# Optimization experiments

Hardware: AMD Instinct MI355X
Metric: run time of the kernel (lower is better)

Reference implementation:

```python
import jax, jax.numpy as jnp
import numpy as np

BERT = 178  # BERT_VECTOR_SIZE
WLEN = 20   # letters per word (dim1 = WLEN + BERT)


def _lstm(x, h0, c0, Wih, Whh, bih, bhh):
    """PyTorch-convention LSTM (gate order i,f,g,o). x: [B,T,D] -> outputs [B,T,H]."""
    xg = jnp.einsum('btd,gd->btg', x, Wih) + bih + bhh  # precompute input projections

    def step(carry, xt):
        h, c = carry
        g = xt + h @ Whh.T
        i, f, gg, o = jnp.split(g, 4, axis=-1)
        c = jax.nn.sigmoid(f) * c + jax.nn.sigmoid(i) * jnp.tanh(gg)
        h = jax.nn.sigmoid(o) * jnp.tanh(c)
        return (h, c), h

    _, hs = jax.lax.scan(step, (h0, c0), jnp.swapaxes(xg, 0, 1))
    return jnp.swapaxes(hs, 0, 1)  # [B,T,H]


def setup_inputs() -> dict:
    key = jax.random.key(0)
    ks = jax.random.split(key, 32)
    B, S, L = 32, 64, 50          # batch, sentence_length, number_of_letters
    Hs, Hm, D, O = 128, 256, 128, 32  # secondary_hidden, main_hidden, word_dims, output_size
    NW = B * S
    T = WLEN + BERT
    Din = D + BERT                # sentence LSTM input size = 306
    s = 0.05
    rn = lambda k, sh: jax.random.normal(k, sh, dtype=jnp.float32)
    return {
        'X': rn(ks[0], (B, S, T, L)),
        'h0w': rn(ks[1], (NW, Hs)), 'c0w': rn(ks[2], (NW, Hs)),
        'h0f': rn(ks[3], (B, Hm)), 'c0f': rn(ks[4], (B, Hm)),
        'h0b': rn(ks[5], (B, Hm)), 'c0b': rn(ks[6], (B, Hm)),
        'Wih_w': rn(ks[7], (4 * Hs, L)) * s, 'Whh_w': rn(ks[8], (4 * Hs, Hs)) * s,
        'bih_w': rn(ks[9], (4 * Hs,)) * s, 'bhh_w': rn(ks[10], (4 * Hs,)) * s,
        'Wl': rn(ks[11], (D, Hs)) * s, 'bl': rn(ks[12], (D,)) * s,
        'Wih_f': rn(ks[13], (4 * Hm, Din)) * s, 'Whh_f': rn(ks[14], (4 * Hm, Hm)) * s,
        'bih_f': rn(ks[15], (4 * Hm,)) * s, 'bhh_f': rn(ks[16], (4 * Hm,)) * s,
        'Wih_b': rn(ks[17], (4 * Hm, Din)) * s, 'Whh_b': rn(ks[18], (4 * Hm, Hm)) * s,
        'bih_b': rn(ks[19], (4 * Hm,)) * s, 'bhh_b': rn(ks[20], (4 * Hm,)) * s,
        'Wo': rn(ks[21], (O, 2 * Hm)) * s, 'bo': rn(ks[22], (O,)) * s,
    }


def reference(X, h0w, c0w, h0f, c0f, h0b, c0b,
              Wih_w, Whh_w, bih_w, bhh_w, Wl, bl,
              Wih_f, Whh_f, bih_f, bhh_f,
              Wih_b, Whh_b, bih_b, bhh_b, Wo, bo):
    B, S = X.shape[0], X.shape[1]
    L = X.shape[-1]
    NW = B * S
    Xw = X.reshape(NW, -1, L)            # [NW, WLEN+BERT, L]
    letters = Xw[:, :WLEN, :]            # [NW, WLEN, L]
    bert = Xw[:, -BERT:, 0]              # vectorized replacement of the double loop

    out_w = _lstm(letters, h0w, c0w, Wih_w, Whh_w, bih_w, bhh_w)
    word_rep = out_w[:, -1, :] @ Wl.T + bl        # [NW, D]
    word_rep = jnp.concatenate([word_rep, bert], axis=1)  # [NW, D+BERT]
    sentences = word_rep.reshape(B, S, -1)

    out_f = _lstm(sentences, h0f, c0f, Wih_f, Whh_f, bih_f, bhh_f)
    out_b = _lstm(sentences[:, ::-1, :], h0b, c0b, Wih_b, Whh_b, bih_b, bhh_b)[:, ::-1, :]
    out = jnp.concatenate([out_f, out_b], axis=-1)  # [B, S, 2*Hm]

    words = out.reshape(NW, -1)
    tags = words @ Wo.T + bo
    return jax.nn.softmax(tags, axis=1)
```

## Files before the change

kernel.cpp:

```cpp
#include <hip/hip_runtime.h>
#include <cstdint>
#include <cstddef>

#define DI static __device__ __forceinline__

using half_t  = _Float16;
using half2_t = __attribute__((ext_vector_type(2))) _Float16;
using half8_t = __attribute__((ext_vector_type(8))) _Float16;
using f32x4_t = __attribute__((ext_vector_type(4))) float;

DI uint32_t pack2(float a, float b){ half2_t h; h[0]=(half_t)a; h[1]=(half_t)b; return __builtin_bit_cast(uint32_t,h); }
DI uint16_t f16b(float a){ return __builtin_bit_cast(uint16_t,(half_t)a); }
DI float lo16(uint32_t u){ half2_t h=__builtin_bit_cast(half2_t,u); return (float)h[0]; }
DI float hi16(uint32_t u){ half2_t h=__builtin_bit_cast(half2_t,u); return (float)h[1]; }
DI float fdot2(uint32_t w, uint32_t x, float acc){
  return __builtin_amdgcn_fdot2(__builtin_bit_cast(half2_t,w), __builtin_bit_cast(half2_t,x), acc, false);
}
DI float sigm(float x){ return __builtin_amdgcn_rcpf(1.f + __expf(-x)); }
DI float tanhf_(float x){ return 1.f - 2.f*__builtin_amdgcn_rcpf(__expf(2.f*x)+1.f); }

#define SROW 308

#define N0 32768
#define N1 16384
#define N2 8192
#define N3 512
#define N4 262144
#define N5 313344
#define N6 2048
#define N7 8192
#define N8 364544
#define NTOT (N0+N1+N2+N3+N4+N5+N6+N7+N8)

__global__ void k_prep(const float* __restrict__ X,
                       const float* __restrict__ Wih_w, const float* __restrict__ Whh_w,
                       const float* __restrict__ bih_w, const float* __restrict__ bhh_w,
                       const float* __restrict__ Wl,
                       const float* __restrict__ Wih_f, const float* __restrict__ Whh_f,
                       const float* __restrict__ bih_f, const float* __restrict__ bhh_f,
                       const float* __restrict__ Wih_b, const float* __restrict__ Whh_b,
                       const float* __restrict__ bih_b, const float* __restrict__ bhh_b,
                       const float* __restrict__ Wo,
                       uint32_t* __restrict__ wWsw, uint32_t* __restrict__ wWxw,
                       uint32_t* __restrict__ wWlf, float* __restrict__ wbsw,
                       uint32_t* __restrict__ wWs, uint32_t* __restrict__ wWihs,
                       float* __restrict__ wbss, uint32_t* __restrict__ wWo,
                       float* __restrict__ sent)
{
  for (int i = blockIdx.x*blockDim.x + threadIdx.x; i < NTOT; i += gridDim.x*blockDim.x) {
    int id = i;
    if (id < N0) {
      int kp = id & 63, ng = id >> 6;
      int w = ng>>6, g = (ng>>4)&3, jl = ng&15;
      const float* s = Whh_w + (size_t)(g*128 + w*16 + jl)*128 + 2*kp;
      wWsw[id] = pack2(s[0], s[1]);
    } else if ((id -= N0) < N1) {
      int kp = id & 31, ng = id >> 5;
      int w = ng>>6, g = (ng>>4)&3, jl = ng&15;
      if (kp < 25) {
        const float* s = Wih_w + (size_t)(g*128 + w*16 + jl)*50 + 2*kp;
        wWxw[id] = pack2(s[0], s[1]);
      } else wWxw[id] = 0u;
    } else if ((id -= N1) < N2) {
      int kp = id & 63, d = id >> 6;
      const float* s = Wl + (size_t)d*128 + 2*kp;
      wWlf[id] = pack2(s[0], s[1]);
    } else if ((id -= N2) < N3) {
      int g = id & 3, j = id>>2;
      wbsw[id] = bih_w[g*128+j] + bhh_w[g*128+j];
    } else if ((id -= N3) < N4) {
      int kp = id & 127, ng = (id>>7)&1023, dir = id>>17;
      int w = ng>>7, g = (ng>>5)&3, jl = ng&31;
      int row = g*256 + w*32 + jl;
      const float* s = (dir ? Whh_b : Whh_f) + (size_t)row*256 + 2*kp;
      wWs[id] = pack2(s[0], s[1]);
    } else if ((id -= N4) < N5) {
      int dir = id >= 156672; int r = id - dir*156672;
      int g = r & 3, j = (r>>2)&255, kp = r>>10;
      const float* s = (dir ? Wih_b : Wih_f) + (size_t)(g*256+j)*306 + 2*kp;
      wWihs[id] = pack2(s[0], s[1]);
    } else if ((id -= N5) < N6) {
      int g = id & 3, j = (id>>2)&255, dir = id>>10;
      int row = g*256+j;
      wbss[id] = dir ? (bih_b[row]+bhh_b[row]) : (bih_f[row]+bhh_f[row]);
    } else if ((id -= N6) < N7) {
      int o = id & 31, kp = id>>5;
      const float* s = Wo + (size_t)o*512 + 2*kp;
      wWo[id] = pack2(s[0], s[1]);
    } else { id -= N7;
      int wg = id / 178, ii = id % 178;
      sent[(size_t)wg*SROW + 128 + ii] = X[(size_t)wg*9900 + (20+ii)*50];
    }
  }
}

__global__ __launch_bounds__(512, 2) void k_word(
    const float* __restrict__ X, const float* __restrict__ h0w, const float* __restrict__ c0w,
    const uint32_t* __restrict__ wWsw, const uint32_t* __restrict__ wWxw,
    const float* __restrict__ wbsw, const uint32_t* __restrict__ wWlf,
    const float* __restrict__ bl, float* __restrict__ sent)
{
  __shared__ __align__(16) uint32_t lets[11520];
  __shared__ __align__(16) uint16_t hbuf[2][2176];
  const int tid = threadIdx.x;
  const int wave = tid >> 6, lane = tid & 63;
  const int l15 = lane & 15, l4 = lane >> 4;
  const int wg0 = blockIdx.x * 16;

  uint4 Bh[4][4], Bx[4][2];
  #pragma unroll
  for (int g = 0; g < 4; ++g) {
    int ng = wave*64 + g*16 + l15;
    #pragma unroll
    for (int Kt = 0; Kt < 4; ++Kt) Bh[g][Kt] = *(const uint4*)(wWsw + ng*64 + Kt*16 + l4*4);
    #pragma unroll
    for (int Kt = 0; Kt < 2; ++Kt) Bx[g][Kt] = *(const uint4*)(wWxw + ng*32 + Kt*16 + l4*4);
  }
  for (int i = tid; i < 11520; i += 512) {
    int c = i % 36, mt = i / 36; int m = mt & 15, t = mt >> 4;
    lets[i] = (c < 25) ? pack2(X[(size_t)(wg0+m)*9900 + t*50 + 2*c],
                               X[(size_t)(wg0+m)*9900 + t*50 + 2*c + 1]) : 0u;
  }
  for (int i = tid; i < 2048; i += 512) {
    int m = i >> 7, k = i & 127;
    hbuf[0][m*136 + k] = f16b(h0w[(size_t)(wg0+m)*128 + k]);
  }
  const float4 bs = *(const float4*)(wbsw + (wave*16 + l15)*4);
  float cr[4];
  #pragma unroll
  for (int r = 0; r < 4; ++r) cr[r] = c0w[(size_t)(wg0 + l4*4 + r)*128 + wave*16 + l15];
  __syncthreads();

  uint16_t* hc = hbuf[0];
  uint16_t* hn = hbuf[1];
  const uint16_t* lp = (const uint16_t*)lets;
  #pragma unroll 1
  for (int t = 0; t < 20; ++t) {
    f32x4_t acc[4];
    acc[0] = (f32x4_t){bs.x,bs.x,bs.x,bs.x};
    acc[1] = (f32x4_t){bs.y,bs.y,bs.y,bs.y};
    acc[2] = (f32x4_t){bs.z,bs.z,bs.z,bs.z};
    acc[3] = (f32x4_t){bs.w,bs.w,bs.w,bs.w};
    #pragma unroll
    for (int Kt = 0; Kt < 2; ++Kt) {
      uint4 av = *(const uint4*)(lp + (t*16 + l15)*72 + Kt*32 + l4*8);
      half8_t a = __builtin_bit_cast(half8_t, av);
      #pragma unroll
      for (int g = 0; g < 4; ++g)
        acc[g] = __builtin_amdgcn_mfma_f32_16x16x32_f16(a, __builtin_bit_cast(half8_t, Bx[g][Kt]), acc[g], 0,0,0);
    }
    #pragma unroll
    for (int Kt = 0; Kt < 4; ++Kt) {
      uint4 av = *(const uint4*)(hc + l15*136 + Kt*32 + l4*8);
      half8_t a = __builtin_bit_cast(half8_t, av);
      #pragma unroll
      for (int g = 0; g < 4; ++g)
        acc[g] = __builtin_amdgcn_mfma_f32_16x16x32_f16(a, __builtin_bit_cast(half8_t, Bh[g][Kt]), acc[g], 0,0,0);
    }
    #pragma unroll
    for (int r = 0; r < 4; ++r) {
      float cc = sigm(acc[1][r])*cr[r] + sigm(acc[0][r])*tanhf_(acc[2][r]);
      cr[r] = cc;
      float hh = sigm(acc[3][r])*tanhf_(cc);
      hn[(l4*4+r)*136 + wave*16 + l15] = f16b(hh);
    }
    uint16_t* tp = hc; hc = hn; hn = tp;
    __syncthreads();
  }
  uint4 Bl[4];
  #pragma unroll
  for (int Kt = 0; Kt < 4; ++Kt) Bl[Kt] = *(const uint4*)(wWlf + (wave*16 + l15)*64 + Kt*16 + l4*4);
  f32x4_t a2 = (f32x4_t){0.f,0.f,0.f,0.f};
  #pragma unroll
  for (int Kt = 0; Kt < 4; ++Kt) {
    uint4 av = *(const uint4*)(hc + l15*136 + Kt*32 + l4*8);
    a2 = __builtin_amdgcn_mfma_f32_16x16x32_f16(__builtin_bit_cast(half8_t, av),
                                                __builtin_bit_cast(half8_t, Bl[Kt]), a2, 0,0,0);
  }
  const float blv = bl[wave*16 + l15];
  #pragma unroll
  for (int r = 0; r < 4; ++r)
    sent[(size_t)(wg0 + l4*4 + r)*SROW + wave*16 + l15] = a2[r] + blv;
}

__global__ __launch_bounds__(256) void k_sxg(
    const float* __restrict__ sent, const uint32_t* __restrict__ Wihs,
    const float* __restrict__ bss, uint2* __restrict__ xgq)
{
  __shared__ uint32_t x16[153*8];
  const int tid = threadIdx.x;
  const int dir = blockIdx.x >> 8, rg = blockIdx.x & 255;
  for (int i = tid; i < 153*8; i += 256) {
    int r = i & 7, kp = i >> 3;
    int ot = rg*8 + r; int b = ot >> 6, tt = ot & 63;
    int si = dir ? (63 - tt) : tt;
    const float* s = sent + (size_t)(b*64 + si)*SROW + 2*kp;
    x16[kp*8 + r] = pack2(s[0], s[1]);
  }
  __syncthreads();
  const int j = tid;
  float acc[8][4];
  {
    const float4 b4 = *(const float4*)(bss + (dir*256 + j)*4);
    #pragma unroll
    for (int r = 0; r < 8; ++r) { acc[r][0]=b4.x; acc[r][1]=b4.y; acc[r][2]=b4.z; acc[r][3]=b4.w; }
  }
  for (int kp = 0; kp < 153; ++kp) {
    uint4 wv = *(const uint4*)(Wihs + ((size_t)(dir*153 + kp)*256 + j)*4);
    uint4 xa = *(const uint4*)(x16 + kp*8);
    uint4 xb = *(const uint4*)(x16 + kp*8 + 4);
    uint32_t wa[4] = {wv.x,wv.y,wv.z,wv.w};
    uint32_t xs[8] = {xa.x,xa.y,xa.z,xa.w,xb.x,xb.y,xb.z,xb.w};
    #pragma unroll
    for (int r = 0; r < 8; ++r)
      #pragma unroll
      for (int g = 0; g < 4; ++g) acc[r][g] = fdot2(wa[g], xs[r], acc[r][g]);
  }
  const int w = j >> 5, jh2 = (j >> 4) & 1, l15j = j & 15;
  #pragma unroll
  for (int r = 0; r < 8; ++r) {
    int ot = rg*8 + r; int b = ot >> 6, tt = ot & 63;
    int half = b >> 4, l4m = (b >> 2) & 3, rm = b & 3;
    uint2 v; v.x = pack2(acc[r][0], acc[r][1]); v.y = pack2(acc[r][2], acc[r][3]);
    size_t idx = ((((size_t)(dir*64 + tt)*2 + half)*8 + w)*2 + jh2)*256 + l15j*16 + l4m*4 + rm;
    xgq[idx] = v;
  }
}

__global__ __launch_bounds__(512, 2) void k_srec(
    const uint32_t* __restrict__ Ws, const float* __restrict__ h0f, const float* __restrict__ c0f,
    const float* __restrict__ h0b, const float* __restrict__ c0b,
    const uint2* __restrict__ xgq, uint16_t* __restrict__ outfb)
{
  extern __shared__ char smem[];
  uint16_t* h16a = (uint16_t*)(smem + 131072);
  uint16_t* h16b = h16a + 4224;
  const int tid = threadIdx.x;
  const int wave = tid >> 6, lane = tid & 63;
  const int dir = blockIdx.x >> 1, half = blockIdx.x & 1, m0 = half * 16;
  const int l15 = lane & 15, l4 = lane >> 4;

  uint4 Breg[8][6];
  #pragma unroll
  for (int Nt = 0; Nt < 8; ++Nt) {
    #pragma unroll
    for (int Kt = 0; Kt < 8; ++Kt) {
      int ng = wave*128 + Nt*16 + l15;
      int kq = Kt*16 + l4*4;
      uint4 v = *(const uint4*)(Ws + (size_t)(dir*1024 + ng)*128 + kq);
      if (Kt < 6) Breg[Nt][Kt] = v;
      else *(uint4*)(smem + (((wave*16 + Nt*2 + (Kt-6))*64 + lane)*16)) = v;
    }
  }
  {
    const float* h0 = dir ? h0b : h0f;
    for (int i = tid; i < 16*256; i += 512) {
      int m = i >> 8, k = i & 255;
      h16a[m*264 + k] = f16b(h0[(size_t)(m0+m)*256 + k]);
    }
  }
  float cr[2][4];
  {
    const float* c0 = dir ? c0b : c0f;
    #pragma unroll
    for (int jh = 0; jh < 2; ++jh)
      #pragma unroll
      for (int r = 0; r < 4; ++r) {
        int m = l4*4 + r, jj = wave*32 + jh*16 + l15;
        cr[jh][r] = c0[(size_t)(m0+m)*256 + jj];
      }
  }
  __syncthreads();

  const char* xb = (const char*)xgq + ((size_t)dir*524288 + (size_t)half*4096)*8;
  const int xoff = wave*4096 + l15*128 + l4*32;
  const int s0 = dir ? 63 : 0, dstep = dir ? -1 : 1;
  uint16_t* op = outfb + ((size_t)(m0 + l4*4)*64 + s0)*512 + dir*256 + wave*32 + l15;

  uint16_t* hc = h16a;
  uint16_t* hn = h16b;
  #pragma unroll 1
  for (int t = 0; t < 64; ++t) {
    #pragma unroll
    for (int jh = 0; jh < 2; ++jh) {
      const char* xbl = xb + (xoff + jh*2048);
      uint4 xga = *(const uint4*)(xbl);
      uint4 xgb = *(const uint4*)(xbl + 16);
      f32x4_t acc[4];
      #pragma unroll
      for (int g = 0; g < 4; ++g) acc[g] = (f32x4_t){0.f,0.f,0.f,0.f};
      #pragma unroll
      for (int Kt = 0; Kt < 8; ++Kt) {
        uint4 av = *(const uint4*)(hc + l15*264 + Kt*32 + l4*8);
        half8_t a = __builtin_bit_cast(half8_t, av);
        #pragma unroll
        for (int g = 0; g < 4; ++g) {
          const int Nt = g*2 + jh;
          uint4 bv = (Kt < 6) ? Breg[Nt][Kt]
                   : *(const uint4*)(smem + (((wave*16 + Nt*2 + (Kt-6))*64 + lane)*16));
          acc[g] = __builtin_amdgcn_mfma_f32_16x16x32_f16(a, __builtin_bit_cast(half8_t, bv), acc[g], 0,0,0);
        }
      }
      #pragma unroll
      for (int r = 0; r < 4; ++r) {
        uint32_t ux = (r==0) ? xga.x : (r==1) ? xga.z : (r==2) ? xgb.x : xgb.z;
        uint32_t uy = (r==0) ? xga.y : (r==1) ? xga.w : (r==2) ? xgb.y : xgb.w;
        float gi = acc[0][r] + lo16(ux);
        float gf = acc[1][r] + hi16(ux);
        float gg = acc[2][r] + lo16(uy);
        float go = acc[3][r] + hi16(uy);
        float ef = __expf(-gf), ei = __expf(-gi), eg = __expf(-2.f*gg);
        float pef = 1.f + ef, pei = 1.f + ei, peg = 1.f + eg;
        float num = cr[jh][r]*pei*peg + (1.f - eg)*pef;
        float cc  = num * __builtin_amdgcn_rcpf(pef*pei*peg);
        cr[jh][r] = cc;
        float ec = __expf(-2.f*cc), eo = __expf(-go);
        float hh = (1.f - ec) * __builtin_amdgcn_rcpf((1.f + ec)*(1.f + eo));
        uint16_t hb = f16b(hh);
        hn[(l4*4+r)*264 + wave*32 + jh*16 + l15] = hb;
        op[(size_t)r*32768 + jh*16] = hb;
      }
      __builtin_amdgcn_sched_barrier(0);
    }
    { uint16_t* tp = hc; hc = hn; hn = tp; }
    xb += 65536;
    op += dstep * 512;
    asm volatile("s_waitcnt lgkmcnt(0)\ns_barrier" ::: "memory");
    __builtin_amdgcn_sched_barrier(0);
  }
}

__global__ __launch_bounds__(256) void k_tags(
    const uint16_t* __restrict__ outfb, const uint32_t* __restrict__ Wo16,
    const float* __restrict__ bo, float* __restrict__ out)
{
  __shared__ uint32_t xr[8*256];
  const int tid = threadIdx.x;
  const int w0 = blockIdx.x * 8;
  const uint32_t* src = (const uint32_t*)outfb;
  for (int i = tid; i < 2048; i += 256) {
    int w = i >> 8, kp = i & 255;
    xr[i] = src[(size_t)(w0+w)*256 + kp];
  }
  __syncthreads();
  const int o = tid & 31, w = tid >> 5;
  float a = bo[o];
  for (int kp = 0; kp < 256; ++kp)
    a = fdot2(Wo16[kp*32 + o], xr[w*256 + kp], a);
  float mx = a;
  #pragma unroll
  for (int off = 16; off; off >>= 1) mx = fmaxf(mx, __shfl_xor(mx, off, 32));
  float e = __expf(a - mx);
  float ssum = e;
  #pragma unroll
  for (int off = 16; off; off >>= 1) ssum += __shfl_xor(ssum, off, 32);
  out[(size_t)(w0+w)*32 + o] = e * __builtin_amdgcn_rcpf(ssum);
}

extern "C" void kernel_launch(void* const* d_in, const int* in_sizes, int n_in,
                              void* d_out, int out_size, void* d_ws, size_t ws_size,
                              hipStream_t stream) {
  const float* X     = (const float*)d_in[0];
  const float* h0w   = (const float*)d_in[1];
  const float* c0w   = (const float*)d_in[2];
  const float* h0f   = (const float*)d_in[3];
  const float* c0f   = (const float*)d_in[4];
  const float* h0b   = (const float*)d_in[5];
  const float* c0b   = (const float*)d_in[6];
  const float* Wih_w = (const float*)d_in[7];
  const float* Whh_w = (const float*)d_in[8];
  const float* bih_w = (const float*)d_in[9];
  const float* bhh_w = (const float*)d_in[10];
  const float* Wl    = (const float*)d_in[11];
  const float* bl    = (const float*)d_in[12];
  const float* Wih_f = (const float*)d_in[13];
  const float* Whh_f = (const float*)d_in[14];
  const float* bih_f = (const float*)d_in[15];
  const float* bhh_f = (const float*)d_in[16];
  const float* Wih_b = (const float*)d_in[17];
  const float* Whh_b = (const float*)d_in[18];
  const float* bih_b = (const float*)d_in[19];
  const float* bhh_b = (const float*)d_in[20];
  const float* Wo    = (const float*)d_in[21];
  const float* bo    = (const float*)d_in[22];

  char* ws = (char*)d_ws;
  uint32_t* wWsw  = (uint32_t*)(ws + 0);
  uint32_t* wWxw  = (uint32_t*)(ws + 131072);
  uint32_t* wWlf  = (uint32_t*)(ws + 196608);
  float*    wbsw  = (float*)   (ws + 229376);
  uint32_t* wWs   = (uint32_t*)(ws + 231424);
  uint32_t* wWihs = (uint32_t*)(ws + 1280000);
  float*    wbss  = (float*)   (ws + 2533376);
  uint32_t* wWo   = (uint32_t*)(ws + 2541568);
  float*    sent  = (float*)   (ws + 2574336);
  uint2*    xgq   = (uint2*)   (ws + 5097472);
  uint16_t* outfb = (uint16_t*)(ws + 13486080);

  hipFuncSetAttribute((const void*)k_srec, hipFuncAttributeMaxDynamicSharedMemorySize, 147968);

  k_prep<<<2048, 256, 0, stream>>>(X, Wih_w, Whh_w, bih_w, bhh_w, Wl, Wih_f, Whh_f, bih_f, bhh_f,
                                   Wih_b, Whh_b, bih_b, bhh_b, Wo,
                                   wWsw, wWxw, wWlf, wbsw, wWs, wWihs, wbss, wWo, sent);
  k_word<<<128, 512, 0, stream>>>(X, h0w, c0w, wWsw, wWxw, wbsw, wWlf, bl, sent);
  k_sxg<<<512, 256, 0, stream>>>(sent, wWihs, wbss, xgq);
  k_srec<<<4, 512, 147968, stream>>>(wWs, h0f, c0f, h0b, c0b, xgq, outfb);
  k_tags<<<256, 256, 0, stream>>>(outfb, wWo, bo, (float*)d_out);
}
```

Measured before the change: 336.0 us.

## Tune sentence LSTM recurrence: padded h stride, xg-initialized accumulators, step-major output layout

Changes the shared-memory row stride of the hidden-state buffer from 264 to 280 halves to cut LDS bank conflicts on the MFMA A-operand loads. The input-gate projections are now loaded at the top of each timestep and used as the MFMA accumulator initial values, which drops the separate adds. The sched_barriers are removed so the compiler can interleave work. The output buffer is relaid out per timestep so the scattered per-step stores are contiguous, and k_tags gathers from the new layout to match. The cost is a strided gather in k_tags and a slightly larger shared allocation.

Measured after the change: 308.3 us. -8.2%, faster.

```diff
diff --git a/kernel.cpp b/kernel.cpp
--- a/kernel.cpp
+++ b/kernel.cpp
@@ -20,6 +20,7 @@
 DI float tanhf_(float x){ return 1.f - 2.f*__builtin_amdgcn_rcpf(__expf(2.f*x)+1.f); }
 
 #define SROW 308
+#define HSTR 280
 
 #define N0 32768
 #define N1 16384
@@ -234,7 +235,7 @@
 {
   extern __shared__ char smem[];
   uint16_t* h16a = (uint16_t*)(smem + 131072);
-  uint16_t* h16b = h16a + 4224;
+  uint16_t* h16b = h16a + 16*HSTR;
   const int tid = threadIdx.x;
   const int wave = tid >> 6, lane = tid & 63;
   const int dir = blockIdx.x >> 1, half = blockIdx.x & 1, m0 = half * 16;
@@ -256,7 +257,7 @@
     const float* h0 = dir ? h0b : h0f;
     for (int i = tid; i < 16*256; i += 512) {
       int m = i >> 8, k = i & 255;
-      h16a[m*264 + k] = f16b(h0[(size_t)(m0+m)*256 + k]);
+      h16a[m*HSTR + k] = f16b(h0[(size_t)(m0+m)*256 + k]);
     }
   }
   float cr[2][4];
@@ -272,26 +273,34 @@
   }
   __syncthreads();
 
-  const char* xb = (const char*)xgq + ((size_t)dir*524288 + (size_t)half*4096)*8;
-  const int xoff = wave*4096 + l15*128 + l4*32;
-  const int s0 = dir ? 63 : 0, dstep = dir ? -1 : 1;
-  uint16_t* op = outfb + ((size_t)(m0 + l4*4)*64 + s0)*512 + dir*256 + wave*32 + l15;
+  const char* xb = (const char*)xgq + ((size_t)dir*4194304 + (size_t)half*32768)
+                 + wave*4096 + l15*128 + l4*32;
+  const int s0 = dir ? 63 : 0;
+  const int sdelta = dir ? -65536 : 65536;
+  char* op = (char*)outfb + (size_t)s0*65536 + half*32768 + dir*16384
+           + (l4*4)*512 + wave*64 + l15*2;
 
   uint16_t* hc = h16a;
   uint16_t* hn = h16b;
   #pragma unroll 1
   for (int t = 0; t < 64; ++t) {
+    uint4 xg0a = *(const uint4*)(xb);
+    uint4 xg0b = *(const uint4*)(xb + 16);
+    uint4 xg1a = *(const uint4*)(xb + 2048);
+    uint4 xg1b = *(const uint4*)(xb + 2048 + 16);
+
     #pragma unroll
     for (int jh = 0; jh < 2; ++jh) {
-      const char* xbl = xb + (xoff + jh*2048);
-      uint4 xga = *(const uint4*)(xbl);
-      uint4 xgb = *(const uint4*)(xbl + 16);
+      const uint4 xga = jh ? xg1a : xg0a;
+      const uint4 xgb = jh ? xg1b : xg0b;
       f32x4_t acc[4];
-      #pragma unroll
-      for (int g = 0; g < 4; ++g) acc[g] = (f32x4_t){0.f,0.f,0.f,0.f};
+      acc[0] = (f32x4_t){lo16(xga.x), lo16(xga.z), lo16(xgb.x), lo16(xgb.z)};
+      acc[1] = (f32x4_t){hi16(xga.x), hi16(xga.z), hi16(xgb.x), hi16(xgb.z)};
+      acc[2] = (f32x4_t){lo16(xga.y), lo16(xga.w), lo16(xgb.y), lo16(xgb.w)};
+      acc[3] = (f32x4_t){hi16(xga.y), hi16(xga.w), hi16(xgb.y), hi16(xgb.w)};
       #pragma unroll
       for (int Kt = 0; Kt < 8; ++Kt) {
-        uint4 av = *(const uint4*)(hc + l15*264 + Kt*32 + l4*8);
+        uint4 av = *(const uint4*)(hc + l15*HSTR + Kt*32 + l4*8);
         half8_t a = __builtin_bit_cast(half8_t, av);
         #pragma unroll
         for (int g = 0; g < 4; ++g) {
@@ -303,12 +312,7 @@
       }
       #pragma unroll
       for (int r = 0; r < 4; ++r) {
-        uint32_t ux = (r==0) ? xga.x : (r==1) ? xga.z : (r==2) ? xgb.x : xgb.z;
-        uint32_t uy = (r==0) ? xga.y : (r==1) ? xga.w : (r==2) ? xgb.y : xgb.w;
-        float gi = acc[0][r] + lo16(ux);
-        float gf = acc[1][r] + hi16(ux);
-        float gg = acc[2][r] + lo16(uy);
-        float go = acc[3][r] + hi16(uy);
+        float gi = acc[0][r], gf = acc[1][r], gg = acc[2][r], go = acc[3][r];
         float ef = __expf(-gf), ei = __expf(-gi), eg = __expf(-2.f*gg);
         float pef = 1.f + ef, pei = 1.f + ei, peg = 1.f + eg;
         float num = cr[jh][r]*pei*peg + (1.f - eg)*pef;
@@ -317,16 +321,14 @@
         float ec = __expf(-2.f*cc), eo = __expf(-go);
         float hh = (1.f - ec) * __builtin_amdgcn_rcpf((1.f + ec)*(1.f + eo));
         uint16_t hb = f16b(hh);
-        hn[(l4*4+r)*264 + wave*32 + jh*16 + l15] = hb;
-        op[(size_t)r*32768 + jh*16] = hb;
+        hn[(l4*4+r)*HSTR + wave*32 + jh*16 + l15] = hb;
+        *(uint16_t*)(op + r*512 + jh*32) = hb;
       }
-      __builtin_amdgcn_sched_barrier(0);
     }
     { uint16_t* tp = hc; hc = hn; hn = tp; }
     xb += 65536;
-    op += dstep * 512;
+    op += sdelta;
     asm volatile("s_waitcnt lgkmcnt(0)\ns_barrier" ::: "memory");
-    __builtin_amdgcn_sched_barrier(0);
   }
 }
 
@@ -340,7 +342,11 @@
   const uint32_t* src = (const uint32_t*)outfb;
   for (int i = tid; i < 2048; i += 256) {
     int w = i >> 8, kp = i & 255;
-    xr[i] = src[(size_t)(w0+w)*256 + kp];
+    int widx = w0 + w;
+    int s = widx & 63, q = widx >> 6;
+    int half = q >> 4, m = q & 15;
+    int dir = kp >> 7, wv = (kp >> 4) & 7, jh = (kp >> 3) & 1, l15h = kp & 7;
+    xr[i] = src[s*16384 + half*8192 + dir*4096 + m*128 + wv*16 + jh*8 + l15h];
   }
   __syncthreads();
   const int o = tid & 31, w = tid >> 5;
@@ -397,13 +403,13 @@
   uint2*    xgq   = (uint2*)   (ws + 5097472);
   uint16_t* outfb = (uint16_t*)(ws + 13486080);
 
-  hipFuncSetAttribute((const void*)k_srec, hipFuncAttributeMaxDynamicSharedMemorySize, 147968);
+  hipFuncSetAttribute((const void*)k_srec, hipFuncAttributeMaxDynamicSharedMemorySize, 148992);
 
   k_prep<<<2048, 256, 0, stream>>>(X, Wih_w, Whh_w, bih_w, bhh_w, Wl, Wih_f, Whh_f, bih_f, bhh_f,
                                    Wih_b, Whh_b, bih_b, bhh_b, Wo,
                                    wWsw, wWxw, wWlf, wbsw, wWs, wWihs, wbss, wWo, sent);
   k_word<<<128, 512, 0, stream>>>(X, h0w, c0w, wWsw, wWxw, wbsw, wWlf, bl, sent);
   k_sxg<<<512, 256, 0, stream>>>(sent, wWihs, wbss, xgq);
-  k_srec<<<4, 512, 147968, stream>>>(wWs, h0f, c0f, h0b, c0b, xgq, outfb);
+  k_srec<<<4, 512, 148992, stream>>>(wWs, h0f, c0f, h0b, c0b, xgq, outfb);
   k_tags<<<256, 256, 0, stream>>>(outfb, wWo, bo, (float*)d_out);
 }
```
